# Optimization experiments

Measured on AMD Instinct MI355X. Metric: run time of the kernel, lower is better.

## Reference

```python
import jax, jax.numpy as jnp
import numpy as np
import math

HIDDEN = 4096
N_HEADS = 32
HEAD_DIM = HIDDEN // N_HEADS
ADAPTER_LEN = 10
BATCH = 1
SEQ = 2048
ROPE_BASE = 10000.0


def setup_inputs() -> dict:
    key = jax.random.key(0)
    ks = jax.random.split(key, 8)
    hidden_states = jax.random.normal(ks[0], (BATCH, SEQ, HIDDEN), dtype=jnp.float32)
    # additive causal mask [B,1,q,kv] with 0 on allowed, large negative on masked
    neg = jnp.finfo(jnp.float32).min
    causal = jnp.triu(jnp.full((SEQ, SEQ), neg, dtype=jnp.float32), k=1)
    attention_mask = jnp.broadcast_to(causal, (BATCH, 1, SEQ, SEQ))
    position_ids = jnp.broadcast_to(jnp.arange(SEQ, dtype=jnp.int64 if jax.config.read('jax_enable_x64') else jnp.int32)[None, :], (BATCH, SEQ))
    s = 0.02
    Wq = jax.random.normal(ks[1], (HIDDEN, HIDDEN), dtype=jnp.float32) * s
    Wk = jax.random.normal(ks[2], (HIDDEN, HIDDEN), dtype=jnp.float32) * s
    Wv = jax.random.normal(ks[3], (HIDDEN, HIDDEN), dtype=jnp.float32) * s
    Wo = jax.random.normal(ks[4], (HIDDEN, HIDDEN), dtype=jnp.float32) * s
    adapter_prefix = jax.random.normal(ks[5], (ADAPTER_LEN, HIDDEN), dtype=jnp.float32) * s
    gate = jnp.zeros((N_HEADS, 1, 1), dtype=jnp.float32) + 0.1  # nonzero so gated path is exercised
    return {"hidden_states": hidden_states, "attention_mask": attention_mask,
            "position_ids": position_ids, "Wq": Wq, "Wk": Wk, "Wv": Wv, "Wo": Wo,
            "adapter_prefix": adapter_prefix, "gate": gate}


def _rotate_half(x):
    x1, x2 = jnp.split(x, 2, axis=-1)
    return jnp.concatenate([-x2, x1], axis=-1)


def _rope_cos_sin(position_ids, head_dim, dtype):
    # inv_freq: [hd/2]
    inv_freq = 1.0 / (ROPE_BASE ** (jnp.arange(0, head_dim, 2, dtype=jnp.float32) / head_dim))
    freqs = position_ids.astype(jnp.float32)[:, :, None] * inv_freq[None, None, :]  # [B,S,hd/2]
    emb = jnp.concatenate([freqs, freqs], axis=-1)  # [B,S,hd]
    cos = jnp.cos(emb)[:, None, :, :].astype(dtype)  # [B,1,S,hd]
    sin = jnp.sin(emb)[:, None, :, :].astype(dtype)
    return cos, sin


def reference(hidden_states, attention_mask, position_ids, Wq, Wk, Wv, Wo, adapter_prefix, gate):
    B, S, H = hidden_states.shape
    nh, hd = N_HEADS, HEAD_DIM
    plen = adapter_prefix.shape[0]

    def proj(x, W):  # torch Linear: x @ W.T
        return jnp.einsum('...h,oh->...o', x, W)

    q = proj(hidden_states, Wq).reshape(B, S, nh, hd).transpose(0, 2, 1, 3)  # [B,nh,S,hd]
    k = proj(hidden_states, Wk).reshape(B, S, nh, hd).transpose(0, 2, 1, 3)
    v = proj(hidden_states, Wv).reshape(B, S, nh, hd).transpose(0, 2, 1, 3)

    cos, sin = _rope_cos_sin(position_ids, hd, q.dtype)
    q = q * cos + _rotate_half(q) * sin
    k = k * cos + _rotate_half(k) * sin

    # adapter prefix KV (bsz must be 1 per original view semantics; no RoPE applied)
    kp = proj(adapter_prefix, Wk).reshape(B, plen, nh, hd).transpose(0, 2, 1, 3)  # [B,nh,plen,hd]
    vp = proj(adapter_prefix, Wv).reshape(B, plen, nh, hd).transpose(0, 2, 1, 3)
    K = jnp.concatenate([kp, k], axis=2)  # [B,nh,plen+S,hd]
    V = jnp.concatenate([vp, v], axis=2)

    mask = jnp.concatenate([jnp.zeros((B, 1, S, plen), dtype=attention_mask.dtype), attention_mask], axis=-1)
    scores = jnp.einsum('bhqd,bhkd->bhqk', q, K) / math.sqrt(hd)
    scores = scores + mask
    scores = jnp.maximum(scores, jnp.finfo(scores.dtype).min)

    prefix_w = jax.nn.softmax(scores[..., :plen].astype(jnp.float32), axis=-1).astype(q.dtype)
    token_w = jax.nn.softmax(scores[..., plen:].astype(jnp.float32), axis=-1).astype(q.dtype)
    g = jnp.tanh(gate)[None, :, :, :]  # [1,nh,1,1]
    attn = jnp.concatenate([g * prefix_w, token_w], axis=-1)  # [B,nh,S,plen+S]

    out = jnp.einsum('bhqk,bhkd->bhqd', attn, V)  # [B,nh,S,hd]
    out = out.transpose(0, 2, 1, 3).reshape(B, S, H)
    return proj(out, Wo)
```

## Files before the change

kernel.cpp:

```cpp
#include <hip/hip_runtime.h>
#include <math.h>

#define HIDDEN 4096
#define NH 32
#define HD 128
#define PLEN 10
#define SEQQ 2048
#define QT 32
#define KT 64
#define QKVLD 12288

typedef __attribute__((ext_vector_type(8))) _Float16 f16x8;
typedef __attribute__((ext_vector_type(4))) float f32x4;

#define GLD16(g, l) __builtin_amdgcn_global_load_lds( \
        (const __attribute__((address_space(1))) void*)(g), \
        (__attribute__((address_space(3))) void*)(l), 16, 0, 0)

__global__ __launch_bounds__(256) void cvt_f16_kernel(
    const float* __restrict__ x, _Float16* __restrict__ y, int n8)
{
    int idx = blockIdx.x * 256 + threadIdx.x;
    if (idx >= n8) return;
    const float4* xp = (const float4*)x;
    float4 a = xp[idx * 2], b = xp[idx * 2 + 1];
    f16x8 o;
    o[0] = (_Float16)a.x; o[1] = (_Float16)a.y; o[2] = (_Float16)a.z; o[3] = (_Float16)a.w;
    o[4] = (_Float16)b.x; o[5] = (_Float16)b.y; o[6] = (_Float16)b.z; o[7] = (_Float16)b.w;
    *(f16x8*)(y + (size_t)idx * 8) = o;
}

__global__ __launch_bounds__(256) void cvt_pad_f16_kernel(
    const float* __restrict__ src, _Float16* __restrict__ y)
{
    int idx = blockIdx.x * 256 + threadIdx.x;
    int row = idx >> 9;
    f16x8 o;
    if (row < PLEN) {
        const float4* xp = (const float4*)src;
        float4 a = xp[idx * 2], b = xp[idx * 2 + 1];
        o[0] = (_Float16)a.x; o[1] = (_Float16)a.y; o[2] = (_Float16)a.z; o[3] = (_Float16)a.w;
        o[4] = (_Float16)b.x; o[5] = (_Float16)b.y; o[6] = (_Float16)b.z; o[7] = (_Float16)b.w;
    } else {
#pragma unroll
        for (int i = 0; i < 8; ++i) o[i] = (_Float16)0.0f;
    }
    *(f16x8*)(y + (size_t)idx * 8) = o;
}

template <typename OT>
__global__ __launch_bounds__(256) void gemm_f16_kernel(
    const _Float16* __restrict__ A, const _Float16* __restrict__ B,
    OT* __restrict__ C, int N, int K, int Mstore)
{
    __shared__ _Float16 lds[2 * 16384];

    const int tid = threadIdx.x;
    const int lane = tid & 63;
    const int wave = tid >> 6;

    const int gx = gridDim.x;
    const int gy = gridDim.y;
    const int nwg = gx * gy;
    const int flat = blockIdx.y * gx + blockIdx.x;
    const int cpx = nwg >> 3;
    const int sw = (flat & 7) * cpx + (flat >> 3);
    const int m0 = (sw % gy) * 128;
    const int n0 = (sw / gy) * 128;

    const _Float16* srcp = (wave < 2) ? A : B;
    const int tb = ((wave < 2) ? m0 : n0) + (wave & 1) * 64;
    const int swz = ((lane & 7) ^ ((lane >> 3) & 7)) << 3;
    const _Float16* p0 = srcp + (size_t)(tb + (lane >> 3)) * K + swz;
    const int ldso = (wave >> 1) * 8192 + (wave & 1) * 4096;

    const int lr = lane & 15;
    const int lq = lane >> 4;
    const int wm = (wave >> 1) * 64;
    const int wn = (wave & 1) * 64;

    f32x4 acc[4][4];
#pragma unroll
    for (int m = 0; m < 4; ++m)
#pragma unroll
        for (int n = 0; n < 4; ++n) acc[m][n] = (f32x4){0.f, 0.f, 0.f, 0.f};

#define STAGE(bufsel, tt) do { \
        _Float16* dst_ = &lds[(bufsel) * 16384 + ldso]; \
        const _Float16* src_ = p0 + ((size_t)(tt) << 6); \
        GLD16(src_ + 0 * 8 * (size_t)K, dst_ + 0 * 512); \
        GLD16(src_ + 1 * 8 * (size_t)K, dst_ + 1 * 512); \
        GLD16(src_ + 2 * 8 * (size_t)K, dst_ + 2 * 512); \
        GLD16(src_ + 3 * 8 * (size_t)K, dst_ + 3 * 512); \
        GLD16(src_ + 4 * 8 * (size_t)K, dst_ + 4 * 512); \
        GLD16(src_ + 5 * 8 * (size_t)K, dst_ + 5 * 512); \
        GLD16(src_ + 6 * 8 * (size_t)K, dst_ + 6 * 512); \
        GLD16(src_ + 7 * 8 * (size_t)K, dst_ + 7 * 512); \
    } while (0)

    const int NK = K >> 6;
    STAGE(0, 0);
    STAGE(1, 1);

    for (int t = 0; t < NK; ++t) {
        const int cur = t & 1;
        if (t == NK - 1) asm volatile("s_waitcnt vmcnt(0)" ::: "memory");
        else             asm volatile("s_waitcnt vmcnt(8)" ::: "memory");
        __builtin_amdgcn_s_barrier();

        const _Float16* la = &lds[cur * 16384];
        const _Float16* lb = &lds[cur * 16384 + 8192];
#pragma unroll
        for (int kc = 0; kc < 2; ++kc) {
            f16x8 af[4], bf[4];
#pragma unroll
            for (int m = 0; m < 4; ++m) {
                int r = wm + m * 16 + lr;
                af[m] = *(const f16x8*)&la[(r << 6) + ((((kc << 2) + lq) ^ (lr & 7)) << 3)];
            }
#pragma unroll
            for (int n = 0; n < 4; ++n) {
                int r = wn + n * 16 + lr;
                bf[n] = *(const f16x8*)&lb[(r << 6) + ((((kc << 2) + lq) ^ (lr & 7)) << 3)];
            }
            __builtin_amdgcn_s_setprio(1);
#pragma unroll
            for (int m = 0; m < 4; ++m)
#pragma unroll
                for (int n = 0; n < 4; ++n)
                    acc[m][n] = __builtin_amdgcn_mfma_f32_16x16x32_f16(af[m], bf[n], acc[m][n], 0, 0, 0);
            __builtin_amdgcn_s_setprio(0);
        }
        __builtin_amdgcn_s_barrier();
        if (t + 2 < NK) STAGE(cur, t + 2);
    }
#undef STAGE

#pragma unroll
    for (int m = 0; m < 4; ++m) {
        const int row = m0 + wm + m * 16 + lq * 4;
#pragma unroll
        for (int n = 0; n < 4; ++n) {
            const int col = n0 + wn + n * 16 + lr;
#pragma unroll
            for (int j = 0; j < 4; ++j)
                if (row + j < Mstore)
                    C[(size_t)(row + j) * N + col] = (OT)acc[m][n][j];
        }
    }
}

__global__ void rope_table_kernel(const int* __restrict__ pos,
                                  float* __restrict__ cosT, float* __restrict__ sinT)
{
    int s = blockIdx.x;
    int j = threadIdx.x;
    float p = (float)pos[s];
    float expnt = (2.0f * (float)j) * (1.0f / 128.0f);
    float inv_freq = powf(10000.0f, -expnt);
    float f = p * inv_freq;
    cosT[s * 64 + j] = cosf(f);
    sinT[s * 64 + j] = sinf(f);
}

__global__ void rope_f16ip_kernel(_Float16* __restrict__ qkv,
                                  const float* __restrict__ cosT, const float* __restrict__ sinT)
{
    int idx = blockIdx.x * 256 + threadIdx.x;
    int s = idx >> 11;
    int rem = idx & 2047;
    int h = rem >> 6;
    int d = rem & 63;
    float c = cosT[s * 64 + d], sn = sinT[s * 64 + d];
    size_t base = (size_t)s * QKVLD + h * HD + d;
    float a = (float)qkv[base], b = (float)qkv[base + 64];
    qkv[base]      = (_Float16)(a * c - b * sn);
    qkv[base + 64] = (_Float16)(b * c + a * sn);
    size_t kb = base + HIDDEN;
    a = (float)qkv[kb]; b = (float)qkv[kb + 64];
    qkv[kb]      = (_Float16)(a * c - b * sn);
    qkv[kb + 64] = (_Float16)(b * c + a * sn);
}

__global__ __launch_bounds__(256) void vtrans_f16_kernel(
    const _Float16* __restrict__ v, _Float16* __restrict__ vt)
{
    __shared__ _Float16 Vsh[64][136];
    const int h = blockIdx.y;
    const int s0 = blockIdx.x * 64;
    const int tid = threadIdx.x;
#pragma unroll
    for (int i = 0; i < 4; ++i) {
        int flat = tid + 256 * i;
        int r = flat >> 4;
        int c8 = (flat & 15) * 8;
        *(f16x8*)&Vsh[r][c8] = *(const f16x8*)(v + (size_t)(s0 + r) * QKVLD + h * HD + c8);
    }
    __syncthreads();
#pragma unroll
    for (int pass = 0; pass < 4; ++pass) {
        int d = pass * 32 + (tid >> 3);
        int sb = (tid & 7) * 8;
        f16x8 o;
#pragma unroll
        for (int e = 0; e < 8; ++e) o[e] = Vsh[sb + e][d];
        *(f16x8*)(vt + ((size_t)h * HD + d) * SEQQ + s0 + sb) = o;
    }
}

__global__ __launch_bounds__(256) void attn_f16_kernel(
    const _Float16* __restrict__ Qf, const _Float16* __restrict__ Kf,
    const _Float16* __restrict__ Vtf,
    const float* __restrict__ kp, const float* __restrict__ vp,
    const float* __restrict__ gate, _Float16* __restrict__ out)
{
    __shared__ _Float16 Ks[64 * 128];
    __shared__ _Float16 Vs[128 * 64];
    __shared__ _Float16 Psh[4][16][72];
    __shared__ float Pp[4][16][12];

    const int h = blockIdx.x;
    const int qt = (gridDim.y - 1) - blockIdx.y;
    const int q0 = qt * 64;
    const int tid = threadIdx.x;
    const int wave = tid >> 6;
    const int lane = tid & 63;
    const int lr = lane & 15;
    const int lq = lane >> 4;
    const float scale = 0.088388347648318447f;
    const float scale2 = 0.088388347648318447f * 1.4426950408889634f;

    const int qrow = q0 + wave * 16 + lr;
    f16x8 qh[4];
#pragma unroll
    for (int c = 0; c < 4; ++c)
        qh[c] = *(const f16x8*)(Qf + (size_t)qrow * QKVLD + h * HD + c * 32 + lq * 8);

    f32x4 accO[8];
#pragma unroll
    for (int n = 0; n < 8; ++n) accO[n] = (f32x4){0.f, 0.f, 0.f, 0.f};
    float m_run[4] = {-INFINITY, -INFINITY, -INFINITY, -INFINITY};
    float l_run[4] = {0.f, 0.f, 0.f, 0.f};

    const int ntiles = qt + 1;
    for (int t = 0; t < ntiles; ++t) {
        const int j0 = t * 64;
        __syncthreads();

        {
            const int rl = lane >> 4;
            const int ch = lane & 15;
#pragma unroll
            for (int ii = 0; ii < 4; ++ii) {
                int r = wave * 16 + ii * 4 + rl;
                int chs = ch ^ (r & 7);
                const _Float16* g = Kf + (size_t)(j0 + r) * QKVLD + h * HD + chs * 8;
                GLD16(g, &Ks[(wave * 16 + ii * 4) * 128]);
            }
        }
        {
            const int dl = lane >> 3;
            const int vch = lane & 7;
#pragma unroll
            for (int ii = 0; ii < 4; ++ii) {
                int d = wave * 32 + ii * 8 + dl;
                int chs = vch ^ (d & 7);
                const _Float16* g = Vtf + ((size_t)h * HD + d) * SEQQ + j0 + chs * 8;
                GLD16(g, &Vs[(wave * 32 + ii * 8) * 64]);
            }
        }
        __syncthreads();

        f32x4 sacc[4];
#pragma unroll
        for (int n = 0; n < 4; ++n) sacc[n] = (f32x4){0.f, 0.f, 0.f, 0.f};
        __builtin_amdgcn_s_setprio(1);
#pragma unroll
        for (int c = 0; c < 4; ++c) {
#pragma unroll
            for (int n = 0; n < 4; ++n) {
                int row = n * 16 + lr;
                int chs = (4 * c + lq) ^ (lr & 7);
                f16x8 kf8 = *(const f16x8*)&Ks[row * 128 + chs * 8];
                sacc[n] = __builtin_amdgcn_mfma_f32_16x16x32_f16(qh[c], kf8, sacc[n], 0, 0, 0);
            }
        }
        __builtin_amdgcn_s_setprio(0);

#pragma unroll
        for (int j = 0; j < 4; ++j) {
            const int grow = q0 + wave * 16 + lq * 4 + j;
#pragma unroll
            for (int n = 0; n < 4; ++n) {
                int gcol = j0 + n * 16 + lr;
                float val = sacc[n][j] * scale2;
                sacc[n][j] = (gcol > grow) ? -INFINITY : val;
            }
            float mx = fmaxf(fmaxf(sacc[0][j], sacc[1][j]), fmaxf(sacc[2][j], sacc[3][j]));
            mx = fmaxf(mx, __shfl_xor(mx, 1));
            mx = fmaxf(mx, __shfl_xor(mx, 2));
            mx = fmaxf(mx, __shfl_xor(mx, 4));
            mx = fmaxf(mx, __shfl_xor(mx, 8));
            float mn = fmaxf(m_run[j], mx);
            float corr = exp2f(m_run[j] - mn);
            m_run[j] = mn;
            float ls = 0.f;
#pragma unroll
            for (int n = 0; n < 4; ++n) {
                float p = exp2f(sacc[n][j] - mn);
                Psh[wave][lq * 4 + j][n * 16 + lr] = (_Float16)p;
                ls += p;
            }
            ls += __shfl_xor(ls, 1);
            ls += __shfl_xor(ls, 2);
            ls += __shfl_xor(ls, 4);
            ls += __shfl_xor(ls, 8);
            l_run[j] = l_run[j] * corr + ls;
#pragma unroll
            for (int n = 0; n < 8; ++n) accO[n][j] *= corr;
        }

        asm volatile("s_waitcnt lgkmcnt(0)" ::: "memory");

        __builtin_amdgcn_s_setprio(1);
#pragma unroll
        for (int jc = 0; jc < 2; ++jc) {
            f16x8 pa = *(const f16x8*)&Psh[wave][lr][jc * 32 + lq * 8];
#pragma unroll
            for (int n = 0; n < 8; ++n) {
                int row = n * 16 + lr;
                int chv = (jc * 4 + lq) ^ (lr & 7);
                f16x8 vf = *(const f16x8*)&Vs[row * 64 + chv * 8];
                accO[n] = __builtin_amdgcn_mfma_f32_16x16x32_f16(pa, vf, accO[n], 0, 0, 0);
            }
        }
        __builtin_amdgcn_s_setprio(0);
    }

#pragma unroll
    for (int j = 0; j < 4; ++j) {
        float inv_l = 1.0f / l_run[j];
#pragma unroll
        for (int n = 0; n < 8; ++n) accO[n][j] *= inv_l;
    }

    {
        float g = tanhf(gate[h]);
        float sp[PLEN];
        float mp = -INFINITY;
#pragma unroll
        for (int i = 0; i < PLEN; ++i) {
            const float* kpr = kp + (size_t)i * QKVLD + h * HD;
            float s = 0.f;
#pragma unroll
            for (int c = 0; c < 4; ++c)
#pragma unroll
                for (int e = 0; e < 8; ++e)
                    s = fmaf((float)qh[c][e], kpr[c * 32 + lq * 8 + e], s);
            s += __shfl_xor(s, 16);
            s += __shfl_xor(s, 32);
            sp[i] = s * scale;
            mp = fmaxf(mp, sp[i]);
        }
        float ssum = 0.f;
#pragma unroll
        for (int i = 0; i < PLEN; ++i) { sp[i] = expf(sp[i] - mp); ssum += sp[i]; }
        float gs = g / ssum;
        if (lq == 0) {
#pragma unroll
            for (int i = 0; i < PLEN; ++i) Pp[wave][lr][i] = sp[i] * gs;
        }
        asm volatile("s_waitcnt lgkmcnt(0)" ::: "memory");
#pragma unroll
        for (int i = 0; i < PLEN; ++i) {
            float vv[8];
#pragma unroll
            for (int n = 0; n < 8; ++n)
                vv[n] = vp[(size_t)i * QKVLD + h * HD + n * 16 + lr];
#pragma unroll
            for (int j = 0; j < 4; ++j) {
                float w = Pp[wave][lq * 4 + j][i];
#pragma unroll
                for (int n = 0; n < 8; ++n) accO[n][j] = fmaf(w, vv[n], accO[n][j]);
            }
        }
    }

#pragma unroll
    for (int n = 0; n < 8; ++n)
#pragma unroll
        for (int j = 0; j < 4; ++j)
            out[(size_t)(q0 + wave * 16 + lq * 4 + j) * HIDDEN + h * HD + n * 16 + lr] =
                (_Float16)accO[n][j];
}

__global__ __launch_bounds__(256) void gemm_nt_kernel(
    const float* __restrict__ A, const float* __restrict__ B, float* __restrict__ C,
    int M, int N, int K)
{
    __shared__ float As[8][132];
    __shared__ float Bs[8][132];
    const int tid = threadIdx.x;
    const int tx = tid & 15, ty = tid >> 4;
    const int m0 = blockIdx.y * 128, n0 = blockIdx.x * 128;
    const int lr = tid >> 1;
    const int lk = (tid & 1) * 4;
    const bool aval = (m0 + lr) < M;
    const float* Ap = A + (size_t)(m0 + lr) * K + lk;
    const float* Bp = B + (size_t)(n0 + lr) * K + lk;

    float acc[8][8];
#pragma unroll
    for (int i = 0; i < 8; ++i)
#pragma unroll
        for (int j = 0; j < 8; ++j) acc[i][j] = 0.0f;

    for (int k0 = 0; k0 < K; k0 += 8) {
        float4 a4 = make_float4(0.f, 0.f, 0.f, 0.f);
        if (aval) a4 = *(const float4*)(Ap + k0);
        float4 b4 = *(const float4*)(Bp + k0);
        __syncthreads();
        As[lk + 0][lr] = a4.x; As[lk + 1][lr] = a4.y; As[lk + 2][lr] = a4.z; As[lk + 3][lr] = a4.w;
        Bs[lk + 0][lr] = b4.x; Bs[lk + 1][lr] = b4.y; Bs[lk + 2][lr] = b4.z; Bs[lk + 3][lr] = b4.w;
        __syncthreads();
#pragma unroll
        for (int kk = 0; kk < 8; ++kk) {
            float4 a0 = *(const float4*)&As[kk][ty * 8];
            float4 a1 = *(const float4*)&As[kk][ty * 8 + 4];
            float4 b0 = *(const float4*)&Bs[kk][tx * 8];
            float4 b1 = *(const float4*)&Bs[kk][tx * 8 + 4];
            float a[8] = {a0.x, a0.y, a0.z, a0.w, a1.x, a1.y, a1.z, a1.w};
            float b[8] = {b0.x, b0.y, b0.z, b0.w, b1.x, b1.y, b1.z, b1.w};
#pragma unroll
            for (int i = 0; i < 8; ++i)
#pragma unroll
                for (int j = 0; j < 8; ++j)
                    acc[i][j] = fmaf(a[i], b[j], acc[i][j]);
        }
    }
#pragma unroll
    for (int i = 0; i < 8; ++i) {
        int row = m0 + ty * 8 + i;
        if (row < M) {
            float* Cp = C + (size_t)row * N + n0 + tx * 8;
            *(float4*)Cp       = make_float4(acc[i][0], acc[i][1], acc[i][2], acc[i][3]);
            *(float4*)(Cp + 4) = make_float4(acc[i][4], acc[i][5], acc[i][6], acc[i][7]);
        }
    }
}

__global__ void rope_apply_kernel(float* __restrict__ q, float* __restrict__ k,
                                  const float* __restrict__ cosT, const float* __restrict__ sinT)
{
    int idx = blockIdx.x * 256 + threadIdx.x;
    int s = idx >> 11;
    int rem = idx & 2047;
    int h = rem >> 6;
    int d = rem & 63;
    float c = cosT[s * 64 + d], sn = sinT[s * 64 + d];
    size_t base = (size_t)s * HIDDEN + h * HD + d;
    float a = q[base], b = q[base + 64];
    q[base]      = a * c - b * sn;
    q[base + 64] = b * c + a * sn;
    a = k[base]; b = k[base + 64];
    k[base]      = a * c - b * sn;
    k[base + 64] = b * c + a * sn;
}

__global__ __launch_bounds__(256) void attn_kernel(
    const float* __restrict__ q, const float* __restrict__ k, const float* __restrict__ v,
    const float* __restrict__ kp, const float* __restrict__ vp,
    const float* __restrict__ gate, float* __restrict__ out)
{
    __shared__ float Qt[128][36];
    __shared__ float KV[128 * 68];
    __shared__ float Psh2[QT][68];

    const int h = blockIdx.y;
    const int r0 = blockIdx.x * QT;
    const int tid = threadIdx.x;
    const int orow = tid >> 3;
    const int oc4 = (tid & 7) * 4;
    const int sy = tid >> 4;
    const int sx = tid & 15;
    const float scale = 0.088388347648318447f;

#pragma unroll
    for (int i = 0; i < 4; ++i) {
        int flat = tid + 256 * i;
        int r = flat >> 5;
        int d = (flat & 31) << 2;
        float4 t = *(const float4*)(q + (size_t)(r0 + r) * HIDDEN + h * HD + d);
        Qt[d + 0][r] = t.x; Qt[d + 1][r] = t.y; Qt[d + 2][r] = t.z; Qt[d + 3][r] = t.w;
    }

    float acc[4][4];
#pragma unroll
    for (int u = 0; u < 4; ++u)
#pragma unroll
        for (int i = 0; i < 4; ++i) acc[u][i] = 0.0f;
    float m_run = -INFINITY, l_run = 0.0f;

    const int jb_max = (r0 + QT - 1) >> 6;
    for (int jb = 0; jb <= jb_max; ++jb) {
        const int j0 = jb * KT;
        __syncthreads();
#pragma unroll
        for (int i = 0; i < 8; ++i) {
            int flat = tid + 256 * i;
            int r = flat >> 5;
            int d = (flat & 31) << 2;
            float4 t = *(const float4*)(k + (size_t)(j0 + r) * HIDDEN + h * HD + d);
            KV[(d + 0) * 68 + r] = t.x; KV[(d + 1) * 68 + r] = t.y;
            KV[(d + 2) * 68 + r] = t.z; KV[(d + 3) * 68 + r] = t.w;
        }
        __syncthreads();
        float s8[2][4] = {{0.f, 0.f, 0.f, 0.f}, {0.f, 0.f, 0.f, 0.f}};
        for (int d = 0; d < 128; ++d) {
            float2 qv = *(const float2*)&Qt[d][sy * 2];
            float4 kv4 = *(const float4*)&KV[d * 68 + sx * 4];
            s8[0][0] = fmaf(qv.x, kv4.x, s8[0][0]);
            s8[0][1] = fmaf(qv.x, kv4.y, s8[0][1]);
            s8[0][2] = fmaf(qv.x, kv4.z, s8[0][2]);
            s8[0][3] = fmaf(qv.x, kv4.w, s8[0][3]);
            s8[1][0] = fmaf(qv.y, kv4.x, s8[1][0]);
            s8[1][1] = fmaf(qv.y, kv4.y, s8[1][1]);
            s8[1][2] = fmaf(qv.y, kv4.z, s8[1][2]);
            s8[1][3] = fmaf(qv.y, kv4.w, s8[1][3]);
        }
#pragma unroll
        for (int i = 0; i < 2; ++i) {
            int gr = r0 + sy * 2 + i;
#pragma unroll
            for (int jj = 0; jj < 4; ++jj) {
                int gj = j0 + sx * 4 + jj;
                float val = s8[i][jj] * scale;
                Psh2[sy * 2 + i][sx * 4 + jj] = (gj > gr) ? -INFINITY : val;
            }
        }
        __syncthreads();
        {
            const int c0 = (tid & 7) * 8;
            float sv[8];
            float mx = -INFINITY;
#pragma unroll
            for (int i = 0; i < 8; ++i) { sv[i] = Psh2[orow][c0 + i]; mx = fmaxf(mx, sv[i]); }
            mx = fmaxf(mx, __shfl_xor(mx, 1));
            mx = fmaxf(mx, __shfl_xor(mx, 2));
            mx = fmaxf(mx, __shfl_xor(mx, 4));
            float m_new = fmaxf(m_run, mx);
            float corr = expf(m_run - m_new);
            float lsum = 0.f;
#pragma unroll
            for (int i = 0; i < 8; ++i) {
                float p = expf(sv[i] - m_new);
                Psh2[orow][c0 + i] = p;
                lsum += p;
            }
            lsum += __shfl_xor(lsum, 1);
            lsum += __shfl_xor(lsum, 2);
            lsum += __shfl_xor(lsum, 4);
            l_run = l_run * corr + lsum;
            m_run = m_new;
#pragma unroll
            for (int u = 0; u < 4; ++u)
#pragma unroll
                for (int i = 0; i < 4; ++i) acc[u][i] *= corr;
        }
        __syncthreads();
#pragma unroll
        for (int i = 0; i < 8; ++i) {
            int flat = tid + 256 * i;
            int r = flat >> 5;
            int d = (flat & 31) << 2;
            float4 t = *(const float4*)(v + (size_t)(j0 + r) * HIDDEN + h * HD + d);
            *(float4*)&KV[r * 136 + d] = t;
        }
        __syncthreads();
        for (int j = 0; j < KT; ++j) {
            float p = Psh2[orow][j];
#pragma unroll
            for (int u = 0; u < 4; ++u) {
                float4 vv = *(const float4*)&KV[j * 136 + oc4 + u * 32];
                acc[u][0] = fmaf(p, vv.x, acc[u][0]);
                acc[u][1] = fmaf(p, vv.y, acc[u][1]);
                acc[u][2] = fmaf(p, vv.z, acc[u][2]);
                acc[u][3] = fmaf(p, vv.w, acc[u][3]);
            }
        }
    }

    float inv_l = 1.0f / l_run;
#pragma unroll
    for (int u = 0; u < 4; ++u)
#pragma unroll
        for (int i = 0; i < 4; ++i) acc[u][i] *= inv_l;

    {
        float g = tanhf(gate[h]);
        float sp[PLEN];
        float mp = -INFINITY;
#pragma unroll
        for (int i = 0; i < PLEN; ++i) {
            const float* kpr = kp + (size_t)i * HIDDEN + h * HD;
            float s = 0.f;
            for (int d = 0; d < 128; ++d) s = fmaf(Qt[d][orow], kpr[d], s);
            sp[i] = s * scale;
            mp = fmaxf(mp, sp[i]);
        }
        float ssum = 0.f;
#pragma unroll
        for (int i = 0; i < PLEN; ++i) { sp[i] = expf(sp[i] - mp); ssum += sp[i]; }
        float gs = g / ssum;
#pragma unroll
        for (int i = 0; i < PLEN; ++i) {
            float w = sp[i] * gs;
            const float* vpr = vp + (size_t)i * HIDDEN + h * HD;
#pragma unroll
            for (int u = 0; u < 4; ++u) {
                float4 vv = *(const float4*)(vpr + oc4 + u * 32);
                acc[u][0] = fmaf(w, vv.x, acc[u][0]);
                acc[u][1] = fmaf(w, vv.y, acc[u][1]);
                acc[u][2] = fmaf(w, vv.z, acc[u][2]);
                acc[u][3] = fmaf(w, vv.w, acc[u][3]);
            }
        }
    }

    float* op = out + (size_t)(r0 + orow) * HIDDEN + h * HD;
#pragma unroll
    for (int u = 0; u < 4; ++u)
        *(float4*)(op + oc4 + u * 32) = make_float4(acc[u][0], acc[u][1], acc[u][2], acc[u][3]);
}

extern "C" void kernel_launch(void* const* d_in, const int* in_sizes, int n_in,
                              void* d_out, int out_size, void* d_ws, size_t ws_size,
                              hipStream_t stream)
{
    (void)in_sizes; (void)n_in; (void)out_size;
    const float* hidden  = (const float*)d_in[0];
    const int*   pos     = (const int*)d_in[2];
    const float* Wq      = (const float*)d_in[3];
    const float* Wk      = (const float*)d_in[4];
    const float* Wv      = (const float*)d_in[5];
    const float* Wo      = (const float*)d_in[6];
    const float* adapter = (const float*)d_in[7];
    const float* gate    = (const float*)d_in[8];
    float* out = (float*)d_out;

    const size_t SH = (size_t)SEQQ * HIDDEN;
    const size_t WN = (size_t)HIDDEN * HIDDEN;
    const size_t PN = (size_t)128 * HIDDEN;

    float* cosT = (float*)d_ws;
    float* sinT = cosT + (size_t)SEQQ * 64;
    float* AP   = sinT + (size_t)SEQQ * 64;
    _Float16* Hf    = (_Float16*)(AP + (size_t)128 * QKVLD);
    _Float16* Wqkvf = Hf + SH;
    _Float16* Pf    = Wqkvf + 3 * WN;
    _Float16* QKVf  = Pf + PN;
    _Float16* Vtf   = QKVf + 3 * SH;
    const size_t need = (size_t)((char*)(Vtf + SH) - (char*)d_ws);
    const bool use_f16 = (ws_size >= need);

    _Float16* Of  = Hf;
    _Float16* Wof = Wqkvf;

    rope_table_kernel<<<SEQQ, 64, 0, stream>>>(pos, cosT, sinT);

    dim3 blk(256);
    const int nH8 = (int)(SH / 8);
    const int nW8 = (int)(WN / 8);

    if (use_f16) {
        cvt_f16_kernel<<<nH8 / 256, blk, 0, stream>>>(hidden, Hf, nH8);
        cvt_f16_kernel<<<nW8 / 256, blk, 0, stream>>>(Wq, Wqkvf, nW8);
        cvt_f16_kernel<<<nW8 / 256, blk, 0, stream>>>(Wk, Wqkvf + WN, nW8);
        cvt_f16_kernel<<<nW8 / 256, blk, 0, stream>>>(Wv, Wqkvf + 2 * WN, nW8);
        cvt_pad_f16_kernel<<<(int)(PN / 8 / 256), blk, 0, stream>>>(adapter, Pf);

        gemm_f16_kernel<_Float16><<<dim3(QKVLD / 128, SEQQ / 128), blk, 0, stream>>>(
            Hf, Wqkvf, QKVf, QKVLD, HIDDEN, SEQQ);
        gemm_f16_kernel<float><<<dim3(QKVLD / 128, 1), blk, 0, stream>>>(
            Pf, Wqkvf, AP, QKVLD, HIDDEN, PLEN);

        rope_f16ip_kernel<<<(SEQQ * 2048) / 256, blk, 0, stream>>>(QKVf, cosT, sinT);
        vtrans_f16_kernel<<<dim3(SEQQ / 64, NH), blk, 0, stream>>>(QKVf + 2 * HIDDEN, Vtf);

        attn_f16_kernel<<<dim3(NH, SEQQ / 64), blk, 0, stream>>>(
            QKVf, QKVf + HIDDEN, Vtf, AP + HIDDEN, AP + 2 * HIDDEN, gate, Of);

        cvt_f16_kernel<<<nW8 / 256, blk, 0, stream>>>(Wo, Wof, nW8);
        gemm_f16_kernel<float><<<dim3(HIDDEN / 128, SEQQ / 128), blk, 0, stream>>>(
            Of, Wof, out, HIDDEN, HIDDEN, SEQQ);
    } else {
        float* ws = (float*)d_ws;
        float* qb   = ws;
        float* kb   = ws + SH;
        float* vb   = ws + 2 * SH;
        float* kpb  = ws + 3 * SH;
        float* vpb  = kpb + (size_t)PLEN * HIDDEN;
        float* cT   = vpb + (size_t)PLEN * HIDDEN;
        float* sT   = cT + (size_t)SEQQ * 64;
        rope_table_kernel<<<SEQQ, 64, 0, stream>>>(pos, cT, sT);
        dim3 gbig(HIDDEN / 128, SEQQ / 128);
        dim3 gsm(HIDDEN / 128, 1);
        gemm_nt_kernel<<<gbig, blk, 0, stream>>>(hidden, Wq, qb, SEQQ, HIDDEN, HIDDEN);
        gemm_nt_kernel<<<gbig, blk, 0, stream>>>(hidden, Wk, kb, SEQQ, HIDDEN, HIDDEN);
        gemm_nt_kernel<<<gbig, blk, 0, stream>>>(hidden, Wv, vb, SEQQ, HIDDEN, HIDDEN);
        gemm_nt_kernel<<<gsm, blk, 0, stream>>>(adapter, Wk, kpb, PLEN, HIDDEN, HIDDEN);
        gemm_nt_kernel<<<gsm, blk, 0, stream>>>(adapter, Wv, vpb, PLEN, HIDDEN, HIDDEN);
        rope_apply_kernel<<<(SEQQ * 2048) / 256, 256, 0, stream>>>(qb, kb, cT, sT);
        attn_kernel<<<dim3(SEQQ / QT, NH), blk, 0, stream>>>(qb, kb, vb, kpb, vpb, gate, qb);
        gemm_nt_kernel<<<gbig, blk, 0, stream>>>(qb, Wo, out, SEQQ, HIDDEN, HIDDEN);
    }
}
```

Before: 553.8 us.

## Add 8-wave 256x128 f16 GEMM with swizzled LDS and split-K double buffering

Adds a new 512-thread GEMM kernel that computes a 256x128 output tile per workgroup with 8 waves. It stages two 32-wide K halves into XOR-swizzled LDS buffers via global_load_lds, double-buffered, and uses setprio around the MFMA blocks. Both the QKV projection and the output projection now use it. The intent is more operand reuse per LDS load and better overlap of loads with MFMA. The cost is higher register and LDS use per workgroup, and half as many workgroups in the grid.

```diff
diff --git a/kernel.cpp b/kernel.cpp
--- a/kernel.cpp
+++ b/kernel.cpp
@@ -16,6 +16,8 @@
 #define GLD16(g, l) __builtin_amdgcn_global_load_lds( \
         (const __attribute__((address_space(1))) void*)(g), \
         (__attribute__((address_space(3))) void*)(l), 16, 0, 0)
+
+__device__ __forceinline__ int swzf(int r) { return (r & 3) ^ ((r >> 2) & 3); }
 
 __global__ __launch_bounds__(256) void cvt_f16_kernel(
     const float* __restrict__ x, _Float16* __restrict__ y, int n8)
@@ -46,6 +48,104 @@
         for (int i = 0; i < 8; ++i) o[i] = (_Float16)0.0f;
     }
     *(f16x8*)(y + (size_t)idx * 8) = o;
+}
+
+template <typename OT>
+__global__ __launch_bounds__(512) void gemm_f16_p8_kernel(
+    const _Float16* __restrict__ A, const _Float16* __restrict__ B,
+    OT* __restrict__ C, int N, int K, int Mstore)
+{
+    __shared__ _Float16 ldsA[2][2][256 * 32];
+    __shared__ _Float16 ldsB[2][2][128 * 32];
+
+    const int tid = threadIdx.x;
+    const int lane = tid & 63;
+    const int wave = tid >> 6;
+
+    const int gx = gridDim.x;
+    const int gy = gridDim.y;
+    const int nwg = gx * gy;
+    const int flat = blockIdx.y * gx + blockIdx.x;
+    const int cpx = nwg >> 3;
+    const int sw = (flat & 7) * cpx + (flat >> 3);
+    const int m0 = (sw % gy) * 256;
+    const int n0 = (sw / gy) * 128;
+
+    const int wr = wave >> 2;
+    const int wc = wave & 3;
+    const int lr = lane & 15;
+    const int lq = lane >> 4;
+
+    const int arow0 = wave * 16 + (lane >> 2);
+    const int arow1 = arow0 + 128;
+    const int acol = ((lane & 3) ^ swzf(arow0)) << 3;
+    const int brow = arow0;
+    const int bcol = acol;
+    const _Float16* gA0 = A + (size_t)(m0 + arow0) * K + acol;
+    const _Float16* gA1 = A + (size_t)(m0 + arow1) * K + acol;
+    const _Float16* gB0 = B + (size_t)(n0 + brow) * K + bcol;
+
+#define STAGE_H(bufsel, hh, tt) do { \
+        const size_t ko_ = ((size_t)(tt) << 6) + ((hh) << 5); \
+        GLD16(gA0 + ko_, &ldsA[bufsel][hh][(size_t)wave * 512]); \
+        GLD16(gA1 + ko_, &ldsA[bufsel][hh][4096 + (size_t)wave * 512]); \
+        GLD16(gB0 + ko_, &ldsB[bufsel][hh][(size_t)wave * 512]); \
+    } while (0)
+
+    const int fslot = (lq ^ swzf(lr)) << 3;
+
+    f32x4 acc[8][2];
+#pragma unroll
+    for (int m = 0; m < 8; ++m)
+#pragma unroll
+        for (int n = 0; n < 2; ++n) acc[m][n] = (f32x4){0.f, 0.f, 0.f, 0.f};
+
+    const int NK = K >> 6;
+    STAGE_H(0, 0, 0);
+    STAGE_H(0, 1, 0);
+
+    for (int k = 0; k < NK; ++k) {
+        const int cur = k & 1;
+        const int nxt = cur ^ 1;
+#pragma unroll
+        for (int kc = 0; kc < 2; ++kc) {
+            if (k == NK - 1 && kc == 1) asm volatile("s_waitcnt vmcnt(0)" ::: "memory");
+            else                        asm volatile("s_waitcnt vmcnt(3)" ::: "memory");
+            __builtin_amdgcn_s_barrier();
+
+            f16x8 af[8], bf[2];
+#pragma unroll
+            for (int m = 0; m < 8; ++m)
+                af[m] = *(const f16x8*)&ldsA[cur][kc][(size_t)(wr * 128 + m * 16 + lr) * 32 + fslot];
+#pragma unroll
+            for (int n = 0; n < 2; ++n)
+                bf[n] = *(const f16x8*)&ldsB[cur][kc][(size_t)(wc * 32 + n * 16 + lr) * 32 + fslot];
+
+            if (k + 1 < NK) STAGE_H(nxt, kc, k + 1);
+
+            __builtin_amdgcn_s_setprio(1);
+#pragma unroll
+            for (int m = 0; m < 8; ++m)
+#pragma unroll
+                for (int n = 0; n < 2; ++n)
+                    acc[m][n] = __builtin_amdgcn_mfma_f32_16x16x32_f16(af[m], bf[n], acc[m][n], 0, 0, 0);
+            __builtin_amdgcn_s_setprio(0);
+        }
+    }
+#undef STAGE_H
+
+#pragma unroll
+    for (int m = 0; m < 8; ++m) {
+        const int row = m0 + wr * 128 + m * 16 + lq * 4;
+#pragma unroll
+        for (int n = 0; n < 2; ++n) {
+            const int col = n0 + wc * 32 + n * 16 + lr;
+#pragma unroll
+            for (int j = 0; j < 4; ++j)
+                if (row + j < Mstore)
+                    C[(size_t)(row + j) * N + col] = (OT)acc[m][n][j];
+        }
+    }
 }
 
 template <typename OT>
@@ -679,7 +779,7 @@
         cvt_f16_kernel<<<nW8 / 256, blk, 0, stream>>>(Wv, Wqkvf + 2 * WN, nW8);
         cvt_pad_f16_kernel<<<(int)(PN / 8 / 256), blk, 0, stream>>>(adapter, Pf);
 
-        gemm_f16_kernel<_Float16><<<dim3(QKVLD / 128, SEQQ / 128), blk, 0, stream>>>(
+        gemm_f16_p8_kernel<_Float16><<<dim3(QKVLD / 128, SEQQ / 256), dim3(512), 0, stream>>>(
             Hf, Wqkvf, QKVf, QKVLD, HIDDEN, SEQQ);
         gemm_f16_kernel<float><<<dim3(QKVLD / 128, 1), blk, 0, stream>>>(
             Pf, Wqkvf, AP, QKVLD, HIDDEN, PLEN);
@@ -691,7 +791,7 @@
             QKVf, QKVf + HIDDEN, Vtf, AP + HIDDEN, AP + 2 * HIDDEN, gate, Of);
 
         cvt_f16_kernel<<<nW8 / 256, blk, 0, stream>>>(Wo, Wof, nW8);
-        gemm_f16_kernel<float><<<dim3(HIDDEN / 128, SEQQ / 128), blk, 0, stream>>>(
+        gemm_f16_p8_kernel<float><<<dim3(HIDDEN / 128, SEQQ / 256), dim3(512), 0, stream>>>(
             Of, Wof, out, HIDDEN, HIDDEN, SEQQ);
     } else {
         float* ws = (float*)d_ws;
```

Measured after the change: 579.5 us. +4.6%, slower.
